# Performance work log

Measured on AMD Instinct MI355X. Metric: run time of the kernel, lower is better.

Reference implementation:

```python
import jax, jax.numpy as jnp
import numpy as np

B, N, D, C, S = 128, 100000, 256, 2000, 751  # batch, memory size, feat dim, num classes, source classes
TEMP = 0.05
EPS = 1e-06


def _l2norm(x):
    return x / jnp.linalg.norm(x, axis=-1, keepdims=True)


def setup_inputs() -> dict:
    key = jax.random.key(0)
    k1, k2, k3, k4, k5 = jax.random.split(key, 5)
    inputs = _l2norm(jax.random.normal(k1, (B, D), dtype=jnp.float32))
    inputs2 = _l2norm(jax.random.normal(k2, (B, D), dtype=jnp.float32))
    features = _l2norm(jax.random.normal(k3, (N, D), dtype=jnp.float32))
    labels = jax.random.randint(k4, (N,), 0, C)
    labels = labels.at[:C].set(jnp.arange(C))  # ensure labels.max()+1 == C
    indexes = jax.random.randint(k5, (B,), 0, N)
    return {"inputs": inputs, "inputs2": inputs2, "features": features,
            "labels": labels, "indexes": indexes, "source_classes": S}


def reference(inputs, inputs2, features, labels, indexes, source_classes):
    # memory-bank logits, [B, N]
    logits = (inputs @ features.T) / TEMP
    logits2 = (inputs2 @ features.T) / TEMP
    targets = labels[indexes]  # [B]

    # per-class counts and segment-mean of logits over the bank, [C, B]
    nums = jax.ops.segment_sum(jnp.ones((N,), jnp.float32), labels, num_segments=C)  # [C]
    denom = jnp.where(nums > 0, nums, 1.0)[:, None]  # [C, 1]
    sim = jax.ops.segment_sum(logits.T, labels, num_segments=C) / denom   # [C, B]
    sim2 = jax.ops.segment_sum(logits2.T, labels, num_segments=C) / denom  # [C, B]

    # MSE between class-probability maps over the first source_classes classes
    p1 = sim[:source_classes].T   # [B, S]
    p2 = sim2[:source_classes].T  # [B, S]
    diff = jax.nn.softmax(p1, axis=1) - jax.nn.softmax(p2, axis=1)
    loss_mse = jnp.sum(diff * diff) / source_classes

    # hard-positive/negative mining: per-class max of logits (0 for empty classes)
    seg_max = jax.ops.segment_max(logits.T, labels, num_segments=C)  # [C, B], -inf where empty
    present = (nums > 0)  # [C]
    sim_hard = jnp.where(present[:, None], seg_max, 0.0).T  # [B, C]
    # for the target class, use the hardest (min) positive instead
    seg_min = jax.ops.segment_min(logits.T, labels, num_segments=C)  # [C, B]
    b_idx = jnp.arange(B)
    sim_hard = sim_hard.at[b_idx, targets].set(seg_min[targets, b_idx])

    # masked softmax over present classes + NLL
    mask = present.astype(jnp.float32)[None, :]  # [1, C]
    exps = jnp.exp(sim_hard) * mask
    masked_sim = exps / (jnp.sum(exps, axis=1, keepdims=True) + EPS)
    loss_con = -jnp.mean(jnp.log(masked_sim[b_idx, targets] + EPS))

    return (loss_con, loss_mse)
```

## Files before the change

kernel.cpp:

```cpp
#include <hip/hip_runtime.h>
#include <hip/hip_bf16.h>

#define BB 128
#define NN 100000
#define DD 256
#define CC 2000
#define SS 751
#define INVTEMP 20.0f
#define EPSV 1e-6f

#define HIST_BLOCKS 391
#define PREP_BLOCKS 32
#define COPY_BLOCKS 3125
#define NTILES_MAX 3563
#define NBLK2 1782

typedef __attribute__((ext_vector_type(8))) short bf16x8;
typedef __attribute__((ext_vector_type(8))) unsigned short u16x8;
typedef __attribute__((ext_vector_type(4))) float f32x4;

__device__ __forceinline__ unsigned short f2bf(float x) {
    unsigned int u = __float_as_uint(x);
    u += 0x7fffu + ((u >> 16) & 1u);
    return (unsigned short)(u >> 16);
}

__device__ __forceinline__ u16x8 pack8(float4 a, float4 b) {
    u16x8 o;
    o[0] = f2bf(a.x); o[1] = f2bf(a.y); o[2] = f2bf(a.z); o[3] = f2bf(a.w);
    o[4] = f2bf(b.x); o[5] = f2bf(b.y); o[6] = f2bf(b.z); o[7] = f2bf(b.w);
    return o;
}

__global__ __launch_bounds__(256) void hist_prep_kernel(
    const int* __restrict__ labels, int* __restrict__ counts,
    const float* __restrict__ in1, const float* __restrict__ in2,
    unsigned short* __restrict__ inb)
{
    int bid = blockIdx.x;
    if (bid < HIST_BLOCKS) {
        int n = bid * 256 + threadIdx.x;
        if (n < NN) atomicAdd(&counts[labels[n]], 1);
    } else {
        int ch = (bid - HIST_BLOCKS) * 256 + threadIdx.x;
        if (ch >= 8192) return;
        int l  = ch & 63;
        int kc = (ch >> 6) & 7;
        int nr = ch >> 9;
        int row = nr * 16 + (l & 15);
        const float* src = (row < BB) ? (in1 + (size_t)row * DD)
                                      : (in2 + (size_t)(row - BB) * DD);
        int k0 = kc * 32 + ((l >> 4) << 3);
        u16x8 o;
        #pragma unroll
        for (int j = 0; j < 8; ++j) o[j] = f2bf(src[k0 + j]);
        *(u16x8*)(inb + (size_t)ch * 8) = o;
    }
}

__global__ __launch_bounds__(256) void scan_kernel(const int* __restrict__ counts,
                                                   int* __restrict__ tile_start,
                                                   int* __restrict__ cursor,
                                                   int* __restrict__ tile_meta,
                                                   int* __restrict__ ntiles_total,
                                                   float* __restrict__ out) {
    const int PT = 8;
    int tid = threadIdx.x;
    if (tid == 0) { out[0] = 0.f; out[1] = 0.f; }
    int tcnt[PT];
    int tot = 0;
    #pragma unroll
    for (int i = 0; i < PT; ++i) {
        int c = tid * PT + i;
        tcnt[i] = (c < CC) ? ((counts[c] + 63) >> 6) : 0;
        tot += tcnt[i];
    }
    __shared__ int sh[256];
    sh[tid] = tot;
    __syncthreads();
    for (int ofs = 1; ofs < 256; ofs <<= 1) {
        int v = (tid >= ofs) ? sh[tid - ofs] : 0;
        __syncthreads();
        sh[tid] += v;
        __syncthreads();
    }
    if (tid == 255) *ntiles_total = sh[255];
    int run = sh[tid] - tot;
    #pragma unroll
    for (int i = 0; i < PT; ++i) {
        int c = tid * PT + i;
        if (c < CC) {
            tile_start[c] = run;
            cursor[c] = run << 6;
            for (int j = 0; j < tcnt[i]; ++j)
                tile_meta[run + j] = (c << 5) | j;
        }
        run += tcnt[i];
    }
}

__global__ __launch_bounds__(256) void scatter_conv(
    const int* __restrict__ labels, int* __restrict__ cursor,
    const float* __restrict__ features, unsigned short* __restrict__ featbf)
{
    int t = blockIdx.x * 256 + threadIdx.x;
    int n = t >> 3;
    int g = t & 7;
    int c = labels[n];
    int p = 0;
    if (g == 0) p = atomicAdd(&cursor[c], 1);
    p = __shfl(p, (threadIdx.x & 63) & ~7, 64);

    const float4* src = (const float4*)(features + (size_t)n * DD) + g * 8;
    unsigned short* dst = featbf + (size_t)p * 256 + g * 32;
    #pragma unroll
    for (int i = 0; i < 4; ++i) {
        float4 a = src[2 * i], b = src[2 * i + 1];
        *(u16x8*)(dst + i * 8) = pack8(a, b);
    }
}

__global__ __launch_bounds__(512, 4) void mm_kernel(
    const unsigned short* __restrict__ featbf, const unsigned short* __restrict__ inb,
    const int* __restrict__ tile_meta, const int* __restrict__ counts,
    const int* __restrict__ ntiles_total,
    float* __restrict__ part_max, float* __restrict__ part_min,
    float* __restrict__ part_sA, float* __restrict__ part_sB)
{
    const int ntt = *ntiles_total;
    const int t0g = 2 * blockIdx.x;
    if (t0g >= ntt) return;
    const int tid = threadIdx.x;
    const int w   = tid >> 6;
    const int l   = tid & 63;

    __shared__ __align__(16) char ldsA[2][32768];

    bf16x8 bfr[16];
    #pragma unroll
    for (int kc = 0; kc < 8; ++kc)
        #pragma unroll
        for (int nb = 0; nb < 2; ++nb) {
            int nr = 2 * w + nb;
            bfr[kc * 2 + nb] = *(const bf16x8*)(inb + (((size_t)(nr * 8 + kc) * 64 + l) << 3));
        }

    const int ntiles_here = min(2, ntt - t0g);
    for (int tt = 0; tt < ntiles_here; ++tt) {
        const char* Abase = (const char*)featbf + ((size_t)(t0g + tt) << 15);
        #pragma unroll
        for (int i = 0; i < 4; ++i) {
            int f   = w * 4 + i;
            int kc  = f & 7;
            int row = ((f >> 3) << 4) + ((l & 15) ^ kc);
            const char* src = Abase + (row << 9) + (kc << 6) + ((l >> 4) << 4);
            __builtin_amdgcn_global_load_lds(
                (const __attribute__((address_space(1))) void*)src,
                (__attribute__((address_space(3))) void*)(&ldsA[tt][0] + (f << 10)),
                16, 0, 0);
        }
    }
    __syncthreads();

    const int h4 = (l >> 4) << 2;
    for (int tt = 0; tt < ntiles_here; ++tt) {
        const int t    = t0g + tt;
        const int meta = tile_meta[t];
        const int c    = meta >> 5;
        const int base_local = (meta & 31) << 6;
        const int cnt  = counts[c];
        const char* L  = &ldsA[tt][0];

        f32x4 acc[4][2];
        #pragma unroll
        for (int ma = 0; ma < 4; ++ma)
            #pragma unroll
            for (int nb = 0; nb < 2; ++nb)
                acc[ma][nb] = (f32x4){0.f, 0.f, 0.f, 0.f};

        __builtin_amdgcn_s_setprio(1);
        #pragma unroll
        for (int kc = 0; kc < 8; ++kc) {
            int lx = (l ^ kc) << 4;
            #pragma unroll
            for (int ma = 0; ma < 4; ++ma) {
                bf16x8 a = *(const bf16x8*)(L + ((ma * 8 + kc) << 10) + lx);
                acc[ma][0] = __builtin_amdgcn_mfma_f32_16x16x32_bf16(a, bfr[kc * 2 + 0], acc[ma][0], 0, 0, 0);
                acc[ma][1] = __builtin_amdgcn_mfma_f32_16x16x32_bf16(a, bfr[kc * 2 + 1], acc[ma][1], 0, 0, 0);
            }
        }
        __builtin_amdgcn_s_setprio(0);

        float sm[2] = {0.f, 0.f};
        float mx[2] = {-3.4e38f, -3.4e38f};
        float mn[2] = { 3.4e38f,  3.4e38f};
        #pragma unroll
        for (int ma = 0; ma < 4; ++ma) {
            #pragma unroll
            for (int reg = 0; reg < 4; ++reg) {
                bool valid = (base_local + 16 * ma + h4 + reg) < cnt;
                if (valid) {
                    #pragma unroll
                    for (int nb = 0; nb < 2; ++nb) {
                        float v = acc[ma][nb][reg];
                        sm[nb] += v;
                        if (w < 4) {
                            mx[nb] = fmaxf(mx[nb], v);
                            mn[nb] = fminf(mn[nb], v);
                        }
                    }
                }
            }
        }
        #pragma unroll
        for (int nb = 0; nb < 2; ++nb) {
            sm[nb] += __shfl_xor(sm[nb], 16);
            sm[nb] += __shfl_xor(sm[nb], 32);
            if (w < 4) {
                mx[nb] = fmaxf(mx[nb], __shfl_xor(mx[nb], 16));
                mx[nb] = fmaxf(mx[nb], __shfl_xor(mx[nb], 32));
                mn[nb] = fminf(mn[nb], __shfl_xor(mn[nb], 16));
                mn[nb] = fminf(mn[nb], __shfl_xor(mn[nb], 32));
            }
        }
        if (l < 16) {
            #pragma unroll
            for (int nb = 0; nb < 2; ++nb) {
                int col = 32 * (w & 3) + 16 * nb + l;
                size_t p = (size_t)t * 128 + col;
                if (w < 4) { part_max[p] = mx[nb]; part_min[p] = mn[nb]; part_sA[p] = sm[nb]; }
                else       { part_sB[p] = sm[nb]; }
            }
        }
    }
}


__device__ __forceinline__ float blk_reduce_sum(float v) {
    __shared__ float sh[4];
    int lane = threadIdx.x & 63, w = threadIdx.x >> 6;
    #pragma unroll
    for (int o = 32; o; o >>= 1) v += __shfl_down(v, o, 64);
    __syncthreads();
    if (lane == 0) sh[w] = v;
    __syncthreads();
    return sh[0] + sh[1] + sh[2] + sh[3];
}

__device__ __forceinline__ float blk_reduce_max(float v) {
    __shared__ float sh[4];
    int lane = threadIdx.x & 63, w = threadIdx.x >> 6;
    #pragma unroll
    for (int o = 32; o; o >>= 1) v = fmaxf(v, __shfl_down(v, o, 64));
    __syncthreads();
    if (lane == 0) sh[w] = v;
    __syncthreads();
    return fmaxf(fmaxf(sh[0], sh[1]), fmaxf(sh[2], sh[3]));
}

__global__ __launch_bounds__(256) void finalize_kernel(
    const float* __restrict__ part_max, const float* __restrict__ part_min,
    const float* __restrict__ part_sA, const float* __restrict__ part_sB,
    const int* __restrict__ tile_start, const int* __restrict__ counts,
    const int* __restrict__ labels, const int* __restrict__ indexes,
    float* __restrict__ out)
{
    const int b   = blockIdx.x;
    const int tid = threadIdx.x;
    const int tgt = labels[indexes[b]];

    __shared__ float a1[SS], a2[SS];
    __shared__ float sh_etgt;

    float local = 0.f;
    for (int c = tid; c < CC; c += 256) {
        int cnt = counts[c];
        if (cnt > 0) {
            int t0 = tile_start[c];
            int nt = (cnt + 63) >> 6;
            bool src = (c < SS);
            float mx = -3.4e38f, sA = 0.f, sB = 0.f;
            for (int j = 0; j < nt; ++j) {
                size_t p = (size_t)(t0 + j) * 128 + b;
                mx = fmaxf(mx, part_max[p]);
                if (src) { sA += part_sA[p]; sB += part_sB[p]; }
            }
            float v = mx;
            if (c == tgt) {
                float mn = 3.4e38f;
                for (int j = 0; j < nt; ++j)
                    mn = fminf(mn, part_min[(size_t)(t0 + j) * 128 + b]);
                v = mn;
            }
            float e = expf(v * INVTEMP);
            local += e;
            if (c == tgt) sh_etgt = e;
            if (src) {
                float icnt = INVTEMP / (float)cnt;
                a1[c] = sA * icnt;
                a2[c] = sB * icnt;
            }
        } else if (c < SS) {
            a1[c] = 0.f;
            a2[c] = 0.f;
        }
    }
    float sum_e = blk_reduce_sum(local);
    float etgt = sh_etgt;
    float loss_con_b = -logf(etgt / (sum_e + EPSV) + EPSV);

    float m1 = -3.4e38f, m2 = -3.4e38f;
    for (int c = tid; c < SS; c += 256) { m1 = fmaxf(m1, a1[c]); m2 = fmaxf(m2, a2[c]); }
    m1 = blk_reduce_max(m1);
    m2 = blk_reduce_max(m2);
    float s1 = 0.f, s2 = 0.f;
    for (int c = tid; c < SS; c += 256) { s1 += expf(a1[c] - m1); s2 += expf(a2[c] - m2); }
    s1 = blk_reduce_sum(s1);
    s2 = blk_reduce_sum(s2);
    float inv1 = 1.f / s1, inv2 = 1.f / s2;
    float dsum = 0.f;
    for (int c = tid; c < SS; c += 256) {
        float d = expf(a1[c] - m1) * inv1 - expf(a2[c] - m2) * inv2;
        dsum += d * d;
    }
    dsum = blk_reduce_sum(dsum);
    if (tid == 0) {
        atomicAdd(&out[0], loss_con_b * (1.0f / (float)BB));
        atomicAdd(&out[1], dsum * (1.0f / (float)SS));
    }
}


extern "C" void kernel_launch(void* const* d_in, const int* in_sizes, int n_in,
                              void* d_out, int out_size, void* d_ws, size_t ws_size,
                              hipStream_t stream) {
    const float* inputs   = (const float*)d_in[0];
    const float* inputs2  = (const float*)d_in[1];
    const float* features = (const float*)d_in[2];
    const int*   labels   = (const int*)d_in[3];
    const int*   indexes  = (const int*)d_in[4];

    float* out = (float*)d_out;

    int* wsi = (int*)d_ws;
    int* counts     = wsi;
    int* tile_start = wsi + 2048;
    int* cursor     = wsi + 4096;
    int* ntiles     = wsi + 6144;
    unsigned short* inb = (unsigned short*)(wsi + 6160);
    int* tile_meta  = wsi + 38928;
    float* part_max = (float*)(wsi + 42496);
    float* part_min = part_max + (size_t)NTILES_MAX * 128;
    float* part_sA  = part_min + (size_t)NTILES_MAX * 128;
    float* part_sB  = part_sA  + (size_t)NTILES_MAX * 128;
    unsigned short* featbf = (unsigned short*)(part_sB + (size_t)NTILES_MAX * 128);

    hipMemsetAsync(counts, 0, 2048 * sizeof(int), stream);

    hist_prep_kernel<<<HIST_BLOCKS + PREP_BLOCKS, 256, 0, stream>>>(
        labels, counts, inputs, inputs2, inb);
    scan_kernel<<<1, 256, 0, stream>>>(counts, tile_start, cursor, tile_meta, ntiles, out);
    scatter_conv<<<COPY_BLOCKS, 256, 0, stream>>>(labels, cursor, features, featbf);
    mm_kernel<<<NBLK2, 512, 0, stream>>>(featbf, inb, tile_meta, counts, ntiles,
                                         part_max, part_min, part_sA, part_sB);
    finalize_kernel<<<BB, 256, 0, stream>>>(part_max, part_min, part_sA, part_sB,
                                            tile_start, counts, labels, indexes, out);
}
```

Baseline: 107.8 us.

## Fuse feature gather and bf16 conversion into matmul via sorted index list

Replaces the scatter_conv pass, which wrote a class-sorted bf16 copy of the feature bank, with a lightweight kernel that scatters only row indices. The matmul kernel then gathers fp32 feature rows directly into LDS by index and converts them to bf16 in registers with packed convert instructions before the MFMAs. This removes a full write and re-read of the converted bank, at the cost of doubling the LDS footprint and the global bytes each tile loads (fp32 rather than bf16), adding conversion ALU work to the inner loop, and moving to one tile per block with the B fragments streamed from memory.

Result: faster. 98.91 us (-8.3%).

```diff
diff --git a/kernel.cpp b/kernel.cpp
--- a/kernel.cpp
+++ b/kernel.cpp
@@ -11,9 +11,7 @@
 
 #define HIST_BLOCKS 391
 #define PREP_BLOCKS 32
-#define COPY_BLOCKS 3125
 #define NTILES_MAX 3563
-#define NBLK2 1782
 
 typedef __attribute__((ext_vector_type(8))) short bf16x8;
 typedef __attribute__((ext_vector_type(8))) unsigned short u16x8;
@@ -25,11 +23,13 @@
     return (unsigned short)(u >> 16);
 }
 
-__device__ __forceinline__ u16x8 pack8(float4 a, float4 b) {
-    u16x8 o;
-    o[0] = f2bf(a.x); o[1] = f2bf(a.y); o[2] = f2bf(a.z); o[3] = f2bf(a.w);
-    o[4] = f2bf(b.x); o[5] = f2bf(b.y); o[6] = f2bf(b.z); o[7] = f2bf(b.w);
-    return o;
+__device__ __forceinline__ bf16x8 cvt8(float4 a, float4 b) {
+    union { unsigned u[4]; bf16x8 v; } cv;
+    asm("v_cvt_pk_bf16_f32 %0, %1, %2" : "=v"(cv.u[0]) : "v"(a.x), "v"(a.y));
+    asm("v_cvt_pk_bf16_f32 %0, %1, %2" : "=v"(cv.u[1]) : "v"(a.z), "v"(a.w));
+    asm("v_cvt_pk_bf16_f32 %0, %1, %2" : "=v"(cv.u[2]) : "v"(b.x), "v"(b.y));
+    asm("v_cvt_pk_bf16_f32 %0, %1, %2" : "=v"(cv.u[3]) : "v"(b.z), "v"(b.w));
+    return cv.v;
 }
 
 __global__ __launch_bounds__(256) void hist_prep_kernel(
@@ -99,138 +99,125 @@
     }
 }
 
-__global__ __launch_bounds__(256) void scatter_conv(
-    const int* __restrict__ labels, int* __restrict__ cursor,
-    const float* __restrict__ features, unsigned short* __restrict__ featbf)
-{
-    int t = blockIdx.x * 256 + threadIdx.x;
-    int n = t >> 3;
-    int g = t & 7;
-    int c = labels[n];
-    int p = 0;
-    if (g == 0) p = atomicAdd(&cursor[c], 1);
-    p = __shfl(p, (threadIdx.x & 63) & ~7, 64);
-
-    const float4* src = (const float4*)(features + (size_t)n * DD) + g * 8;
-    unsigned short* dst = featbf + (size_t)p * 256 + g * 32;
-    #pragma unroll
-    for (int i = 0; i < 4; ++i) {
-        float4 a = src[2 * i], b = src[2 * i + 1];
-        *(u16x8*)(dst + i * 8) = pack8(a, b);
+__global__ void scatter_idx(const int* __restrict__ labels, int* __restrict__ cursor,
+                            int* __restrict__ sorted_idx) {
+    int n = blockIdx.x * 256 + threadIdx.x;
+    if (n < NN) {
+        int c = labels[n];
+        int p = atomicAdd(&cursor[c], 1);
+        sorted_idx[p] = n;
     }
 }
 
 __global__ __launch_bounds__(512, 4) void mm_kernel(
-    const unsigned short* __restrict__ featbf, const unsigned short* __restrict__ inb,
-    const int* __restrict__ tile_meta, const int* __restrict__ counts,
-    const int* __restrict__ ntiles_total,
+    const float* __restrict__ features, const unsigned short* __restrict__ inb,
+    const int* __restrict__ sorted_idx, const int* __restrict__ tile_meta,
+    const int* __restrict__ counts, const int* __restrict__ ntiles_total,
     float* __restrict__ part_max, float* __restrict__ part_min,
     float* __restrict__ part_sA, float* __restrict__ part_sB)
 {
-    const int ntt = *ntiles_total;
-    const int t0g = 2 * blockIdx.x;
-    if (t0g >= ntt) return;
+    const int t = blockIdx.x;
+    if (t >= *ntiles_total) return;
     const int tid = threadIdx.x;
     const int w   = tid >> 6;
     const int l   = tid & 63;
-
-    __shared__ __align__(16) char ldsA[2][32768];
-
-    bf16x8 bfr[16];
-    #pragma unroll
-    for (int kc = 0; kc < 8; ++kc)
-        #pragma unroll
-        for (int nb = 0; nb < 2; ++nb) {
-            int nr = 2 * w + nb;
-            bfr[kc * 2 + nb] = *(const bf16x8*)(inb + (((size_t)(nr * 8 + kc) * 64 + l) << 3));
-        }
-
-    const int ntiles_here = min(2, ntt - t0g);
-    for (int tt = 0; tt < ntiles_here; ++tt) {
-        const char* Abase = (const char*)featbf + ((size_t)(t0g + tt) << 15);
-        #pragma unroll
-        for (int i = 0; i < 4; ++i) {
-            int f   = w * 4 + i;
-            int kc  = f & 7;
-            int row = ((f >> 3) << 4) + ((l & 15) ^ kc);
-            const char* src = Abase + (row << 9) + (kc << 6) + ((l >> 4) << 4);
-            __builtin_amdgcn_global_load_lds(
-                (const __attribute__((address_space(1))) void*)src,
-                (__attribute__((address_space(3))) void*)(&ldsA[tt][0] + (f << 10)),
-                16, 0, 0);
-        }
-    }
-    __syncthreads();
+    const int meta = tile_meta[t];
+    const int base_local = (meta & 31) << 6;
+    const int cnt  = counts[meta >> 5];
+    const int vrows = cnt - base_local;
+
+    __shared__ __align__(16) char ldsF[65536];
+
+    #pragma unroll
+    for (int i2 = 0; i2 < 8; ++i2) {
+        int row = w * 8 + i2;
+        int idx = t * 64 + ((row < vrows) ? row : 0);
+        int n   = sorted_idx[idx];
+        const float* src = features + (size_t)n * DD + ((l ^ (row & 7)) << 2);
+        __builtin_amdgcn_global_load_lds(
+            (const __attribute__((address_space(1))) void*)src,
+            (__attribute__((address_space(3))) void*)(&ldsF[0] + (row << 10)),
+            16, 0, 0);
+    }
+    __syncthreads();
+
+    f32x4 acc[4][2];
+    #pragma unroll
+    for (int ma = 0; ma < 4; ++ma)
+        #pragma unroll
+        for (int nb = 0; nb < 2; ++nb)
+            acc[ma][nb] = (f32x4){0.f, 0.f, 0.f, 0.f};
+
+    const int rlow = l & 15;
+    const int cbase = (l >> 4) << 1;
+
+    bf16x8 bcur0 = *(const bf16x8*)(inb + (((size_t)((2 * w + 0) * 8 + 0) * 64 + l) << 3));
+    bf16x8 bcur1 = *(const bf16x8*)(inb + (((size_t)((2 * w + 1) * 8 + 0) * 64 + l) << 3));
+
+    __builtin_amdgcn_s_setprio(1);
+    #pragma unroll
+    for (int kc = 0; kc < 8; ++kc) {
+        bf16x8 bnx0 = bcur0, bnx1 = bcur1;
+        if (kc < 7) {
+            bnx0 = *(const bf16x8*)(inb + (((size_t)((2 * w + 0) * 8 + kc + 1) * 64 + l) << 3));
+            bnx1 = *(const bf16x8*)(inb + (((size_t)((2 * w + 1) * 8 + kc + 1) * 64 + l) << 3));
+        }
+        #pragma unroll
+        for (int ma = 0; ma < 4; ++ma) {
+            int r  = 16 * ma + rlow;
+            int x  = r & 7;
+            int c0 = kc * 8 + cbase;
+            const char* Lr = &ldsF[0] + (r << 10);
+            float4 f0 = *(const float4*)(Lr + (((c0    ) ^ x) << 4));
+            float4 f1 = *(const float4*)(Lr + (((c0 + 1) ^ x) << 4));
+            bf16x8 a = cvt8(f0, f1);
+            acc[ma][0] = __builtin_amdgcn_mfma_f32_16x16x32_bf16(a, bcur0, acc[ma][0], 0, 0, 0);
+            acc[ma][1] = __builtin_amdgcn_mfma_f32_16x16x32_bf16(a, bcur1, acc[ma][1], 0, 0, 0);
+        }
+        bcur0 = bnx0; bcur1 = bnx1;
+    }
+    __builtin_amdgcn_s_setprio(0);
 
     const int h4 = (l >> 4) << 2;
-    for (int tt = 0; tt < ntiles_here; ++tt) {
-        const int t    = t0g + tt;
-        const int meta = tile_meta[t];
-        const int c    = meta >> 5;
-        const int base_local = (meta & 31) << 6;
-        const int cnt  = counts[c];
-        const char* L  = &ldsA[tt][0];
-
-        f32x4 acc[4][2];
-        #pragma unroll
-        for (int ma = 0; ma < 4; ++ma)
-            #pragma unroll
-            for (int nb = 0; nb < 2; ++nb)
-                acc[ma][nb] = (f32x4){0.f, 0.f, 0.f, 0.f};
-
-        __builtin_amdgcn_s_setprio(1);
-        #pragma unroll
-        for (int kc = 0; kc < 8; ++kc) {
-            int lx = (l ^ kc) << 4;
-            #pragma unroll
-            for (int ma = 0; ma < 4; ++ma) {
-                bf16x8 a = *(const bf16x8*)(L + ((ma * 8 + kc) << 10) + lx);
-                acc[ma][0] = __builtin_amdgcn_mfma_f32_16x16x32_bf16(a, bfr[kc * 2 + 0], acc[ma][0], 0, 0, 0);
-                acc[ma][1] = __builtin_amdgcn_mfma_f32_16x16x32_bf16(a, bfr[kc * 2 + 1], acc[ma][1], 0, 0, 0);
-            }
-        }
-        __builtin_amdgcn_s_setprio(0);
-
-        float sm[2] = {0.f, 0.f};
-        float mx[2] = {-3.4e38f, -3.4e38f};
-        float mn[2] = { 3.4e38f,  3.4e38f};
-        #pragma unroll
-        for (int ma = 0; ma < 4; ++ma) {
-            #pragma unroll
-            for (int reg = 0; reg < 4; ++reg) {
-                bool valid = (base_local + 16 * ma + h4 + reg) < cnt;
-                if (valid) {
-                    #pragma unroll
-                    for (int nb = 0; nb < 2; ++nb) {
-                        float v = acc[ma][nb][reg];
-                        sm[nb] += v;
-                        if (w < 4) {
-                            mx[nb] = fmaxf(mx[nb], v);
-                            mn[nb] = fminf(mn[nb], v);
-                        }
+    float sm[2] = {0.f, 0.f};
+    float mx[2] = {-3.4e38f, -3.4e38f};
+    float mn[2] = { 3.4e38f,  3.4e38f};
+    #pragma unroll
+    for (int ma = 0; ma < 4; ++ma) {
+        #pragma unroll
+        for (int reg = 0; reg < 4; ++reg) {
+            bool valid = (16 * ma + h4 + reg) < vrows;
+            if (valid) {
+                #pragma unroll
+                for (int nb = 0; nb < 2; ++nb) {
+                    float v = acc[ma][nb][reg];
+                    sm[nb] += v;
+                    if (w < 4) {
+                        mx[nb] = fmaxf(mx[nb], v);
+                        mn[nb] = fminf(mn[nb], v);
                     }
                 }
             }
         }
+    }
+    #pragma unroll
+    for (int nb = 0; nb < 2; ++nb) {
+        sm[nb] += __shfl_xor(sm[nb], 16);
+        sm[nb] += __shfl_xor(sm[nb], 32);
+        if (w < 4) {
+            mx[nb] = fmaxf(mx[nb], __shfl_xor(mx[nb], 16));
+            mx[nb] = fmaxf(mx[nb], __shfl_xor(mx[nb], 32));
+            mn[nb] = fminf(mn[nb], __shfl_xor(mn[nb], 16));
+            mn[nb] = fminf(mn[nb], __shfl_xor(mn[nb], 32));
+        }
+    }
+    if (l < 16) {
         #pragma unroll
         for (int nb = 0; nb < 2; ++nb) {
-            sm[nb] += __shfl_xor(sm[nb], 16);
-            sm[nb] += __shfl_xor(sm[nb], 32);
-            if (w < 4) {
-                mx[nb] = fmaxf(mx[nb], __shfl_xor(mx[nb], 16));
-                mx[nb] = fmaxf(mx[nb], __shfl_xor(mx[nb], 32));
-                mn[nb] = fminf(mn[nb], __shfl_xor(mn[nb], 16));
-                mn[nb] = fminf(mn[nb], __shfl_xor(mn[nb], 32));
-            }
-        }
-        if (l < 16) {
-            #pragma unroll
-            for (int nb = 0; nb < 2; ++nb) {
-                int col = 32 * (w & 3) + 16 * nb + l;
-                size_t p = (size_t)t * 128 + col;
-                if (w < 4) { part_max[p] = mx[nb]; part_min[p] = mn[nb]; part_sA[p] = sm[nb]; }
-                else       { part_sB[p] = sm[nb]; }
-            }
+            int col = 32 * (w & 3) + 16 * nb + l;
+            size_t p = (size_t)t * 128 + col;
+            if (w < 4) { part_max[p] = mx[nb]; part_min[p] = mn[nb]; part_sA[p] = sm[nb]; }
+            else       { part_sB[p] = sm[nb]; }
         }
     }
 }
@@ -349,20 +336,21 @@
     int* ntiles     = wsi + 6144;
     unsigned short* inb = (unsigned short*)(wsi + 6160);
     int* tile_meta  = wsi + 38928;
-    float* part_max = (float*)(wsi + 42496);
+    int* sorted_idx = wsi + 42496;
+    float* part_max = (float*)(wsi + 270592);
     float* part_min = part_max + (size_t)NTILES_MAX * 128;
     float* part_sA  = part_min + (size_t)NTILES_MAX * 128;
     float* part_sB  = part_sA  + (size_t)NTILES_MAX * 128;
-    unsigned short* featbf = (unsigned short*)(part_sB + (size_t)NTILES_MAX * 128);
 
     hipMemsetAsync(counts, 0, 2048 * sizeof(int), stream);
 
     hist_prep_kernel<<<HIST_BLOCKS + PREP_BLOCKS, 256, 0, stream>>>(
         labels, counts, inputs, inputs2, inb);
     scan_kernel<<<1, 256, 0, stream>>>(counts, tile_start, cursor, tile_meta, ntiles, out);
-    scatter_conv<<<COPY_BLOCKS, 256, 0, stream>>>(labels, cursor, features, featbf);
-    mm_kernel<<<NBLK2, 512, 0, stream>>>(featbf, inb, tile_meta, counts, ntiles,
-                                         part_max, part_min, part_sA, part_sB);
+    scatter_idx<<<HIST_BLOCKS, 256, 0, stream>>>(labels, cursor, sorted_idx);
+    mm_kernel<<<NTILES_MAX, 512, 0, stream>>>(features, inb, sorted_idx, tile_meta,
+                                              counts, ntiles,
+                                              part_max, part_min, part_sA, part_sB);
     finalize_kernel<<<BB, 256, 0, stream>>>(part_max, part_min, part_sA, part_sB,
                                             tile_start, counts, labels, indexes, out);
 }
```
